# Performance work log

Measured on AMD Instinct MI355X. Metric: run time of the kernel, lower is better.

## Reference

```python
import jax, jax.numpy as jnp
import numpy as np

L = 2          # conv layers
N = 50000      # nodes
E = 800000     # edges (before self loops)
F_IN = 256     # raw node features
C = 32         # embed features (out_channels per head)
H = 4          # heads
HC = H * C
ED = 1         # edge feature dim
EPS = 1e-5
NEG_SLOPE = 0.2


def _xavier(k, shape):
    fan_in, fan_out = shape[-2], shape[-1]
    lim = float(np.sqrt(6.0 / (fan_in + fan_out)))
    return jax.random.uniform(k, shape, jnp.float32, -lim, lim)


def setup_inputs() -> dict:
    key = jax.random.key(0)
    ks = jax.random.split(key, 12)
    x = jax.random.normal(ks[0], (N, F_IN), jnp.float32)
    src = jax.random.randint(ks[1], (E,), 0, N, dtype=jnp.int32)
    off = jax.random.randint(ks[2], (E,), 1, N, dtype=jnp.int32)
    dst = (src + off) % N  # guarantees no pre-existing self loops (PyG removes then re-adds them)
    edge_index = jnp.stack([src, dst])
    edge_attr = jax.random.normal(ks[3], (E, ED), jnp.float32)
    return {
        "x": x,
        "edge_index": edge_index,
        "edge_attr": edge_attr,
        "W_emb": _xavier(ks[4], (F_IN, C)),
        "b_emb": jnp.zeros((C,), jnp.float32),
        "ln0_w": jnp.ones((C,), jnp.float32),
        "ln0_b": jnp.zeros((C,), jnp.float32),
        "Wl": _xavier(ks[5], (L, C, HC)),
        "bl": jnp.zeros((L, HC), jnp.float32),
        "Wr": _xavier(ks[6], (L, C, HC)),
        "br": jnp.zeros((L, HC), jnp.float32),
        "We": _xavier(ks[7], (L, ED, HC)),
        "att": jax.random.normal(ks[8], (L, H, C), jnp.float32) * 0.1,
        "gat_b": jnp.zeros((L, HC), jnp.float32),
        "ln1_w": jnp.ones((L, HC), jnp.float32),
        "ln1_b": jnp.zeros((L, HC), jnp.float32),
        "lin_w": _xavier(ks[9], (L, HC, C)),
        "lin_b": jnp.zeros((L, C), jnp.float32),
        "ln2_w": jnp.ones((L, C), jnp.float32),
        "ln2_b": jnp.zeros((L, C), jnp.float32),
    }


def _node_ln(x, w, b):
    # torch.nn.LayerNorm over last dim
    mu = jnp.mean(x, axis=-1, keepdims=True)
    xc = x - mu
    var = jnp.mean(xc * xc, axis=-1, keepdims=True)
    return xc / jnp.sqrt(var + EPS) * w + b


def _graph_ln(x, w, b):
    # torch_geometric.nn.norm.LayerNorm, mode='graph': normalize over ALL nodes+features
    mu = jnp.mean(x)
    xc = x - mu
    var = jnp.mean(xc * xc)
    return xc / jnp.sqrt(var + EPS) * w + b


def _gatv2_layer(h, src, dst, ea, Wl, bl, Wr, br, We, att, gat_b):
    n = h.shape[0]
    xl = (h @ Wl + bl).reshape(n, H, C)   # lin_l(x) -> source transform
    xr = (h @ Wr + br).reshape(n, H, C)   # lin_r(x) -> target transform
    e = (ea @ We).reshape(-1, H, C)       # lin_edge(edge_attr), no bias
    z = jax.nn.leaky_relu(xl[src] + xr[dst] + e, NEG_SLOPE)   # [Etot,H,C]
    logits = jnp.einsum("ehc,hc->eh", z, att)                  # [Etot,H]
    # segment softmax over destination nodes (every node has a self loop)
    m = jax.ops.segment_max(logits, dst, num_segments=n)
    ex = jnp.exp(logits - m[dst])
    s = jax.ops.segment_sum(ex, dst, num_segments=n)
    alpha = ex / s[dst]                                        # [Etot,H]
    msg = alpha[..., None] * xl[src]                           # [Etot,H,C]
    out = jax.ops.segment_sum(msg, dst, num_segments=n)        # [N,H,C]
    return out.reshape(n, HC) + gat_b


def reference(x, edge_index, edge_attr, W_emb, b_emb, ln0_w, ln0_b, Wl, bl, Wr, br,
              We, att, gat_b, ln1_w, ln1_b, lin_w, lin_b, ln2_w, ln2_b):
    n = x.shape[0]
    loop = jnp.arange(n, dtype=edge_index.dtype)
    src = jnp.concatenate([edge_index[0], loop])
    dst = jnp.concatenate([edge_index[1], loop])
    ea = jnp.concatenate([edge_attr, jnp.zeros((n, edge_attr.shape[1]), edge_attr.dtype)])  # fill_value=0.0

    # node_embed: Dropout(eval=identity) -> Linear -> LayerNorm -> ReLU
    h = jax.nn.relu(_node_ln(x @ W_emb + b_emb, ln0_w, ln0_b))
    hs = [h]
    for i in range(L):
        g = _gatv2_layer(h, src, dst, ea, Wl[i], bl[i], Wr[i], br[i], We[i], att[i], gat_b[i])
        g = jax.nn.relu(_graph_ln(g, ln1_w[i], ln1_b[i]))     # PyG graph-mode LayerNorm + ReLU
        g = g @ lin_w[i] + lin_b[i]                            # heads>1 projection back to C
        h = jax.nn.relu(_node_ln(g, ln2_w[i], ln2_b[i]))
        hs.append(h)
    # JumpingKnowledge mode='max': elementwise max over layer outputs
    return jnp.max(jnp.stack(hs, axis=0), axis=0)
```

## Files before the change

kernel.cpp:

```cpp
#include <hip/hip_runtime.h>
#include <hip/hip_fp16.h>

constexpr int kNodes = 50000;
constexpr int kNE    = 800000;
constexpr int kFin   = 256;
constexpr int kC     = 32;
constexpr int kH     = 4;
constexpr int kHC    = 128;
constexpr int kTN    = 16;
constexpr int kLWP   = 130;
constexpr int kEmbedBlocks = kNodes / kTN;
constexpr int kTransBlocks = (kNodes + 31) / 32;
constexpr int kHistGS = 256;
constexpr int kReoGS  = 256;
constexpr int kDegBlocks = (kNodes + 255) / 256;
constexpr float kEps   = 1e-5f;
constexpr float kSlope = 0.2f;
constexpr float kL2E   = 1.44269504f;
constexpr float kShift2 = 8.0f * 1.44269504f;

typedef _Float16 f16;
typedef _Float16 f16x2 __attribute__((ext_vector_type(2)));
struct alignas(16) h8 { f16x2 v[4]; };

__device__ __forceinline__ float fdot2_(f16x2 a, f16x2 b, float c) {
#if __has_builtin(__builtin_amdgcn_fdot2)
    return __builtin_amdgcn_fdot2(a, b, c, false);
#else
    return fmaf((float)a.x, (float)b.x, fmaf((float)a.y, (float)b.y, c));
#endif
}

template<int CTRL>
__device__ __forceinline__ float dpp_add(float v) {
    int x = __builtin_amdgcn_update_dpp(0, __float_as_int(v), CTRL, 0xF, 0xF, true);
    return v + __int_as_float(x);
}
__device__ __forceinline__ float red8(float p) {
    p = dpp_add<0xB1>(p);
    p = dpp_add<0x4E>(p);
    p = dpp_add<0x141>(p);
    return p;
}

__global__ void __launch_bounds__(256) k_prep(
    unsigned* __restrict__ deg, const float* __restrict__ W, f16* __restrict__ Wh) {
    int t = threadIdx.x;
    if (blockIdx.x < kDegBlocks) {
        int i = blockIdx.x * 256 + t;
        if (i < kNodes) deg[i] = 0u;
        return;
    }
    int i = (blockIdx.x - kDegBlocks) * 256 + t;
    int k = i >> 5, c = i & 31;
    Wh[((k >> 3) * kC + c) * 8 + (k & 7)] = (f16)W[i];
}

__global__ void __launch_bounds__(256) k_embed_hist(
    const float* __restrict__ x, const f16* __restrict__ Wh, const float* __restrict__ b,
    const float* __restrict__ lnw, const float* __restrict__ lnb,
    float* __restrict__ h, float* __restrict__ jk,
    const int* __restrict__ dst, int* __restrict__ deg, unsigned short* __restrict__ rank) {
    __shared__ f16 sxh[kTN * kFin];
    __shared__ f16 sWh[kFin / 8 * kC * 8];
    int t = threadIdx.x;
    if (blockIdx.x < kHistGS) {
        const int stride = kHistGS * 256;
        int e = blockIdx.x * 256 + t;
        for (; e + 3 * stride < kNE; e += 4 * stride) {
            int d0 = dst[e], d1 = dst[e + stride], d2 = dst[e + 2 * stride], d3 = dst[e + 3 * stride];
            int r0 = atomicAdd(&deg[d0], 1);
            int r1 = atomicAdd(&deg[d1], 1);
            int r2 = atomicAdd(&deg[d2], 1);
            int r3 = atomicAdd(&deg[d3], 1);
            rank[e] = (unsigned short)r0;
            rank[e + stride] = (unsigned short)r1;
            rank[e + 2 * stride] = (unsigned short)r2;
            rank[e + 3 * stride] = (unsigned short)r3;
        }
        for (; e < kNE; e += stride) {
            int d = dst[e];
            rank[e] = (unsigned short)atomicAdd(&deg[d], 1);
        }
        return;
    }
    int n0 = (blockIdx.x - kHistGS) * kTN;
    {
        const h8* Wg = (const h8*)Wh;
        h8* sW8 = (h8*)sWh;
        for (int i = t; i < kFin * kC / 8; i += 256) sW8[i] = Wg[i];
    }
    const float2* xg2 = (const float2*)(x + (long)n0 * kFin);
    f16x2* sx2 = (f16x2*)sxh;
    for (int i = t; i < kTN * kFin / 2; i += 256) {
        float2 v = xg2[i];
        f16x2 hv; hv.x = (f16)v.x; hv.y = (f16)v.y;
        sx2[i] = hv;
    }
    __syncthreads();
    int c = t & 31, n2 = t >> 5;
    const h8* xa = (const h8*)(sxh + n2 * kFin);
    const h8* xb = (const h8*)(sxh + (n2 + 8) * kFin);
    const h8* wr = (const h8*)sWh;
    float a0 = 0.f, a0b = 0.f, a1 = 0.f, a1b = 0.f;
    #pragma unroll 8
    for (int i8 = 0; i8 < kFin / 8; ++i8) {
        h8 xv0 = xa[i8];
        h8 xv1 = xb[i8];
        h8 wv  = wr[i8 * kC + c];
        a0  = fdot2_(xv0.v[0], wv.v[0], a0);
        a0b = fdot2_(xv0.v[1], wv.v[1], a0b);
        a0  = fdot2_(xv0.v[2], wv.v[2], a0);
        a0b = fdot2_(xv0.v[3], wv.v[3], a0b);
        a1  = fdot2_(xv1.v[0], wv.v[0], a1);
        a1b = fdot2_(xv1.v[1], wv.v[1], a1b);
        a1  = fdot2_(xv1.v[2], wv.v[2], a1);
        a1b = fdot2_(xv1.v[3], wv.v[3], a1b);
    }
    float acc0 = a0 + a0b, acc1 = a1 + a1b;
    float bc = b[c], lw = lnw[c], lb = lnb[c];
    {
        float y = acc0 + bc;
        float m = y;
        #pragma unroll
        for (int o = 1; o < 32; o <<= 1) m += __shfl_xor(m, o);
        m *= (1.f / kC);
        float xc = y - m, v = xc * xc;
        #pragma unroll
        for (int o = 1; o < 32; o <<= 1) v += __shfl_xor(v, o);
        v *= (1.f / kC);
        float out = fmaxf(xc * rsqrtf(v + kEps) * lw + lb, 0.f);
        int node = n0 + n2;
        h[node * kC + c] = out;
        jk[node * kC + c] = out;
    }
    {
        float y = acc1 + bc;
        float m = y;
        #pragma unroll
        for (int o = 1; o < 32; o <<= 1) m += __shfl_xor(m, o);
        m *= (1.f / kC);
        float xc = y - m, v = xc * xc;
        #pragma unroll
        for (int o = 1; o < 32; o <<= 1) v += __shfl_xor(v, o);
        v *= (1.f / kC);
        float out = fmaxf(xc * rsqrtf(v + kEps) * lw + lb, 0.f);
        int node = n0 + n2 + 8;
        h[node * kC + c] = out;
        jk[node * kC + c] = out;
    }
}

__device__ __forceinline__ void trans_body(
    int bid, float* s_h, const float* __restrict__ h,
    const float* __restrict__ Wl, const float* __restrict__ bl,
    const float* __restrict__ Wr, const float* __restrict__ br,
    __half* __restrict__ xl, float* __restrict__ xr) {
    int t = threadIdx.x;
    int j = t & 127, hf = t >> 7;
    float wl[kC], wr[kC];
    #pragma unroll
    for (int k = 0; k < kC; ++k) { wl[k] = Wl[k * kHC + j]; wr[k] = Wr[k * kHC + j]; }
    float blj = bl[j], brj = br[j];
    int n0 = bid * 32;
    int nn = min(32, kNodes - n0);
    for (int i = t; i < nn * kC; i += 256) s_h[i] = h[n0 * kC + i];
    __syncthreads();
    int nend = min(nn, hf * 16 + 16);
    for (int n = hf * 16; n < nend; ++n) {
        const float4* h4 = (const float4*)(s_h + n * kC);
        float al = blj, ar = brj;
        #pragma unroll
        for (int kq = 0; kq < 8; ++kq) {
            float4 hv = h4[kq];
            al += hv.x * wl[kq*4] + hv.y * wl[kq*4+1] + hv.z * wl[kq*4+2] + hv.w * wl[kq*4+3];
            ar += hv.x * wr[kq*4] + hv.y * wr[kq*4+1] + hv.z * wr[kq*4+2] + hv.w * wr[kq*4+3];
        }
        long g = (long)(n0 + n) * kHC + j;
        xl[g] = __float2half(al);
        xr[g] = ar;
    }
}

__global__ void __launch_bounds__(256) k_trans(
    const float* __restrict__ h,
    const float* __restrict__ Wl, const float* __restrict__ bl,
    const float* __restrict__ Wr, const float* __restrict__ br,
    __half* __restrict__ xl, float* __restrict__ xr, float* __restrict__ stats) {
    __shared__ float s_h[32 * kC];
    if (blockIdx.x == 0 && threadIdx.x == 0) { stats[0] = 0.f; stats[1] = 0.f; }
    trans_body(blockIdx.x, s_h, h, Wl, bl, Wr, br, xl, xr);
}

__global__ void __launch_bounds__(256) k_trans_reorder(
    const float* __restrict__ h,
    const float* __restrict__ Wl, const float* __restrict__ bl,
    const float* __restrict__ Wr, const float* __restrict__ br,
    __half* __restrict__ xl, float* __restrict__ xr,
    const int* __restrict__ src, const int* __restrict__ dst, const float* __restrict__ ea,
    const int* __restrict__ rowptr, const unsigned short* __restrict__ rank,
    int2* __restrict__ epack, float* __restrict__ stats) {
    __shared__ float s_h[32 * kC];
    if (blockIdx.x < kReoGS) {
        const int stride = kReoGS * 256;
        int e = blockIdx.x * 256 + threadIdx.x;
        for (; e + 3 * stride < kNE; e += 4 * stride) {
            int e1 = e + stride, e2 = e + 2 * stride, e3 = e + 3 * stride;
            int d0 = dst[e], d1 = dst[e1], d2 = dst[e2], d3 = dst[e3];
            int r0 = rank[e], r1 = rank[e1], r2 = rank[e2], r3 = rank[e3];
            int p0 = rowptr[d0] + r0, p1 = rowptr[d1] + r1;
            int p2 = rowptr[d2] + r2, p3 = rowptr[d3] + r3;
            epack[p0] = make_int2(src[e],  __float_as_int(ea[e]));
            epack[p1] = make_int2(src[e1], __float_as_int(ea[e1]));
            epack[p2] = make_int2(src[e2], __float_as_int(ea[e2]));
            epack[p3] = make_int2(src[e3], __float_as_int(ea[e3]));
        }
        for (; e < kNE; e += stride) {
            int d = dst[e];
            int pos = rowptr[d] + (int)rank[e];
            epack[pos] = make_int2(src[e], __float_as_int(ea[e]));
        }
        return;
    }
    if (blockIdx.x == kReoGS && threadIdx.x == 0) { stats[0] = 0.f; stats[1] = 0.f; }
    trans_body(blockIdx.x - kReoGS, s_h, h, Wl, bl, Wr, br, xl, xr);
}

__global__ void __launch_bounds__(256) k_scan1(const int* __restrict__ deg,
                                               int* __restrict__ excl, int* __restrict__ bsum) {
    __shared__ int s[256];
    int t = threadIdx.x;
    int i = blockIdx.x * 256 + t;
    int v = (i < kNodes) ? deg[i] : 0;
    s[t] = v;
    __syncthreads();
    for (int o = 1; o < 256; o <<= 1) {
        int tv = (t >= o) ? s[t - o] : 0;
        __syncthreads();
        s[t] += tv;
        __syncthreads();
    }
    if (i < kNodes) excl[i] = s[t] - v;
    if (t == 255) bsum[blockIdx.x] = s[255];
}

__global__ void __launch_bounds__(256) k_scan2(int* __restrict__ bsum, int nb) {
    __shared__ int s[256];
    int t = threadIdx.x;
    int v = (t < nb) ? bsum[t] : 0;
    s[t] = v;
    __syncthreads();
    for (int o = 1; o < 256; o <<= 1) {
        int tv = (t >= o) ? s[t - o] : 0;
        __syncthreads();
        s[t] += tv;
        __syncthreads();
    }
    if (t < nb) bsum[t] = s[t];
}

__global__ void __launch_bounds__(256) k_scan3(int* __restrict__ excl, const int* __restrict__ bsum) {
    int i = blockIdx.x * 256 + threadIdx.x;
    if (i >= kNodes) return;
    if (blockIdx.x > 0) excl[i] += bsum[blockIdx.x - 1];
}

struct h4 { __half2 a, b; };
template<int U>
__device__ __forceinline__ void gat_batch(
    const int2* __restrict__ epack, int base2, bool slot0, int f,
    const h4* __restrict__ xl4, float4 Wev, float4 xrv, float4 av,
    float& l, float& o0, float& o1, float& o2, float& o3) {
    int2 pa[U], pb[U];
    #pragma unroll
    for (int u = 0; u < U; ++u) {
        pa[u] = epack[base2 + 2 * u];
        pb[u] = epack[base2 + 2 * u + 1];
    }
    h4 xv[U]; float eav[U];
    #pragma unroll
    for (int u = 0; u < U; ++u) {
        int srow = slot0 ? pa[u].x : pb[u].x;
        xv[u] = xl4[(long)srow * 32 + f];
        eav[u] = __int_as_float(slot0 ? pa[u].y : pb[u].y);
    }
    #pragma unroll
    for (int u = 0; u < U; ++u) {
        float2 x01 = __half22float2(xv[u].a), x23 = __half22float2(xv[u].b);
        float a0 = fmaf(eav[u], Wev.x, xrv.x) + x01.x;
        float a1 = fmaf(eav[u], Wev.y, xrv.y) + x01.y;
        float a2 = fmaf(eav[u], Wev.z, xrv.z) + x23.x;
        float a3 = fmaf(eav[u], Wev.w, xrv.w) + x23.y;
        a0 = fmaxf(a0, kSlope * a0); a1 = fmaxf(a1, kSlope * a1);
        a2 = fmaxf(a2, kSlope * a2); a3 = fmaxf(a3, kSlope * a3);
        float pp = red8(a0 * av.x + a1 * av.y + a2 * av.z + a3 * av.w);
        float eu = __builtin_amdgcn_exp2f(pp - kShift2);
        l += eu;
        o0 = fmaf(eu, x01.x, o0); o1 = fmaf(eu, x01.y, o1);
        o2 = fmaf(eu, x23.x, o2); o3 = fmaf(eu, x23.y, o3);
    }
}

__global__ void __launch_bounds__(256) k_edge(
    const int* __restrict__ rowptr, const int* __restrict__ deg,
    const int2* __restrict__ epack,
    const __half* __restrict__ xl, float* __restrict__ xrg,
    const float* __restrict__ We, const float* __restrict__ att,
    const float* __restrict__ gat_b, float* __restrict__ ps, float* __restrict__ pq) {
    int t = threadIdx.x & 63;
    int w = __builtin_amdgcn_readfirstlane(threadIdx.x >> 6);
    int d = blockIdx.x * 4 + w;
    int f = t & 31;
    bool slot0 = (t < 32);
    float em0 = slot0 ? 1.f : 0.f;

    const h4* xl4 = (const h4*)xl;
    long rowq = (long)d * 32;

    float4 xrv = ((const float4*)xrg)[rowq + f];
    float4 Wev = ((const float4*)We)[f];
    float4 av  = ((const float4*)att)[f];
    av.x *= kL2E; av.y *= kL2E; av.z *= kL2E; av.w *= kL2E;
    float4 gb  = ((const float4*)gat_b)[f];

    h4 xs = xl4[rowq + f];
    float2 xs01 = __half22float2(xs.a), xs23 = __half22float2(xs.b);

    float z0 = xs01.x + xrv.x, z1 = xs01.y + xrv.y;
    float z2 = xs23.x + xrv.z, z3 = xs23.y + xrv.w;
    z0 = fmaxf(z0, kSlope * z0); z1 = fmaxf(z1, kSlope * z1);
    z2 = fmaxf(z2, kSlope * z2); z3 = fmaxf(z3, kSlope * z3);
    float p = red8(z0 * av.x + z1 * av.y + z2 * av.z + z3 * av.w);
    float ee = __builtin_amdgcn_exp2f(p - kShift2) * em0;
    float l = ee;
    float o0 = ee * xs01.x, o1 = ee * xs01.y, o2 = ee * xs23.x, o3 = ee * xs23.y;

    int base = rowptr[d], cnt = deg[d];
    int npair = cnt >> 1;
    int e = 0;
    for (; e + 8 <= npair; e += 8)
        gat_batch<8>(epack, base + 2 * e, slot0, f, xl4, Wev, xrv, av, l, o0, o1, o2, o3);
    if (e + 4 <= npair) {
        gat_batch<4>(epack, base + 2 * e, slot0, f, xl4, Wev, xrv, av, l, o0, o1, o2, o3);
        e += 4;
    }
    for (; e < npair; ++e)
        gat_batch<1>(epack, base + 2 * e, slot0, f, xl4, Wev, xrv, av, l, o0, o1, o2, o3);
    if (cnt & 1) {
        int2 ep = epack[base + cnt - 1];
        int srow = ep.x;
        float eav = __int_as_float(ep.y);
        h4 xv = xl4[(long)srow * 32 + f];
        float2 x01 = __half22float2(xv.a), x23 = __half22float2(xv.b);
        float a0 = fmaf(eav, Wev.x, xrv.x) + x01.x;
        float a1 = fmaf(eav, Wev.y, xrv.y) + x01.y;
        float a2 = fmaf(eav, Wev.z, xrv.z) + x23.x;
        float a3 = fmaf(eav, Wev.w, xrv.w) + x23.y;
        a0 = fmaxf(a0, kSlope * a0); a1 = fmaxf(a1, kSlope * a1);
        a2 = fmaxf(a2, kSlope * a2); a3 = fmaxf(a3, kSlope * a3);
        float pp = red8(a0 * av.x + a1 * av.y + a2 * av.z + a3 * av.w);
        float eu = __builtin_amdgcn_exp2f(pp - kShift2) * em0;
        l += eu;
        o0 = fmaf(eu, x01.x, o0); o1 = fmaf(eu, x01.y, o1);
        o2 = fmaf(eu, x23.x, o2); o3 = fmaf(eu, x23.y, o3);
    }
    l  += __shfl_xor(l, 32);
    o0 += __shfl_xor(o0, 32); o1 += __shfl_xor(o1, 32);
    o2 += __shfl_xor(o2, 32); o3 += __shfl_xor(o3, 32);
    float rl = __builtin_amdgcn_rcpf(l);
    float v0 = o0 * rl, v1 = o1 * rl, v2 = o2 * rl, v3 = o3 * rl;
    if (slot0)
        ((float4*)xrg)[rowq + f] = make_float4(v0, v1, v2, v3);
    float vb0 = v0 + gb.x, vb1 = v1 + gb.y, vb2 = v2 + gb.z, vb3 = v3 + gb.w;
    float s = vb0 + vb1 + vb2 + vb3;
    float q = vb0 * vb0 + vb1 * vb1 + vb2 * vb2 + vb3 * vb3;
    #pragma unroll
    for (int mm = 1; mm < 32; mm <<= 1) { s += __shfl_xor(s, mm); q += __shfl_xor(q, mm); }
    if (t == 0) { ps[d] = s; pq[d] = q; }
}

__global__ void __launch_bounds__(1024) k_statsr(
    const float* __restrict__ ps, const float* __restrict__ pq, float* __restrict__ stats) {
    __shared__ float rs[1024], rq[1024];
    int t = threadIdx.x;
    float s = 0.f, q = 0.f;
    for (int i = blockIdx.x * 1024 + t; i < kNodes; i += 8 * 1024) { s += ps[i]; q += pq[i]; }
    rs[t] = s; rq[t] = q;
    __syncthreads();
    for (int o = 512; o > 0; o >>= 1) {
        if (t < o) { rs[t] += rs[t + o]; rq[t] += rq[t + o]; }
        __syncthreads();
    }
    if (t == 0) { atomicAdd(&stats[0], rs[0]); atomicAdd(&stats[1], rq[0]); }
}

__global__ void __launch_bounds__(256) k_post(
    const float* __restrict__ g, const float* __restrict__ gat_b,
    const float* __restrict__ ln1w, const float* __restrict__ ln1b,
    const float* __restrict__ linw, const float* __restrict__ linb,
    const float* __restrict__ ln2w, const float* __restrict__ ln2b,
    const float* __restrict__ stats, const float* __restrict__ jk_in,
    float* __restrict__ h, float* __restrict__ jk_out) {
    __shared__ float s_lwT[kC * kLWP];
    __shared__ float s_vb[8 * kHC];
    int t = threadIdx.x;
    int n0 = blockIdx.x * 8;
    const float inv = 1.f / ((float)kNodes * kHC);
    float mean = stats[0] * inv;
    float var  = stats[1] * inv - mean * mean;
    float rstd = rsqrtf(var + kEps);
    for (int i = t; i < kHC * kC; i += 256) {
        int k = i >> 5, c = i & 31;
        s_lwT[c * kLWP + k] = linw[i];
    }
    for (int i = t; i < 8 * kHC; i += 256) {
        int node = n0 + (i >> 7), f = i & 127;
        float a = (g[(long)node * kHC + f] + gat_b[f] - mean) * rstd * ln1w[f] + ln1b[f];
        s_vb[i] = fmaxf(a, 0.f);
    }
    __syncthreads();
    int n = t >> 5, c = t & 31;
    int node = n0 + n;
    float acc = linb[c];
    const float* vb = s_vb + n * kHC;
    const float* wr = s_lwT + c * kLWP;
    #pragma unroll 8
    for (int k = 0; k < kHC; k += 4) {
        float4 v4 = *(const float4*)(vb + k);
        float2 w0 = *(const float2*)(wr + k);
        float2 w1 = *(const float2*)(wr + k + 2);
        acc += v4.x * w0.x + v4.y * w0.y + v4.z * w1.x + v4.w * w1.y;
    }
    float m = acc;
    #pragma unroll
    for (int mm = 1; mm < 32; mm <<= 1) m += __shfl_xor(m, mm);
    m *= (1.f / kC);
    float dd = acc - m;
    float q = dd * dd;
    #pragma unroll
    for (int mm = 1; mm < 32; mm <<= 1) q += __shfl_xor(q, mm);
    q *= (1.f / kC);
    float out = dd * rsqrtf(q + kEps) * ln2w[c] + ln2b[c];
    out = fmaxf(out, 0.f);
    h[node * kC + c] = out;
    jk_out[node * kC + c] = fmaxf(jk_in[node * kC + c], out);
}

extern "C" void kernel_launch(void* const* d_in, const int* in_sizes, int n_in,
                              void* d_out, int out_size, void* d_ws, size_t ws_size,
                              hipStream_t stream) {
    (void)in_sizes; (void)n_in; (void)out_size; (void)ws_size;
    const float* x     = (const float*)d_in[0];
    const int*   ei    = (const int*)d_in[1];
    const int*   src   = ei;
    const int*   dst   = ei + kNE;
    const float* ea    = (const float*)d_in[2];
    const float* W_emb = (const float*)d_in[3];
    const float* b_emb = (const float*)d_in[4];
    const float* ln0w  = (const float*)d_in[5];
    const float* ln0b  = (const float*)d_in[6];
    const float* Wl    = (const float*)d_in[7];
    const float* bl    = (const float*)d_in[8];
    const float* Wr    = (const float*)d_in[9];
    const float* br    = (const float*)d_in[10];
    const float* We    = (const float*)d_in[11];
    const float* att   = (const float*)d_in[12];
    const float* gat_b = (const float*)d_in[13];
    const float* ln1w  = (const float*)d_in[14];
    const float* ln1b  = (const float*)d_in[15];
    const float* linw  = (const float*)d_in[16];
    const float* linb  = (const float*)d_in[17];
    const float* ln2w  = (const float*)d_in[18];
    const float* ln2b  = (const float*)d_in[19];

    char* wsb = (char*)d_ws;
    float*  h      = (float*)(wsb);
    float*  jk     = (float*)(wsb +  6400000);
    float*  xrg    = (float*)(wsb + 12800000);
    __half* xl     = (__half*)(wsb + 38400000);
    int2*   epack  = (int2*)(wsb + 51200000);
    int*    deg    = (int*)(wsb + 57600000);
    int*    rowptr = (int*)(wsb + 58000000);
    int*    bsum   = (int*)(wsb + 58200000);
    float*  stats  = (float*)(wsb + 58201024);
    float*  ps     = (float*)(wsb + 58300000);
    float*  pq     = (float*)(wsb + 58500000);
    unsigned short* rank = (unsigned short*)(wsb + 58700000);
    f16*    Wh     = (f16*)(wsb + 60400000);

    const int scanBlocks = (kNodes + 255) / 256;
    const int edgeBlocks = kNodes / 4;
    const int postBlocks = kNodes / 8;

    hipLaunchKernelGGL(k_prep, dim3(kDegBlocks + 32), dim3(256), 0, stream,
                       (unsigned*)deg, W_emb, Wh);
    hipLaunchKernelGGL(k_embed_hist, dim3(kHistGS + kEmbedBlocks), dim3(256), 0, stream,
                       x, Wh, b_emb, ln0w, ln0b, h, jk, dst, deg, rank);
    hipLaunchKernelGGL(k_scan1, dim3(scanBlocks), dim3(256), 0, stream, deg, rowptr, bsum);
    hipLaunchKernelGGL(k_scan2, dim3(1), dim3(256), 0, stream, bsum, scanBlocks);
    hipLaunchKernelGGL(k_scan3, dim3(scanBlocks), dim3(256), 0, stream, rowptr, bsum);
    hipLaunchKernelGGL(k_trans_reorder, dim3(kReoGS + kTransBlocks), dim3(256), 0, stream,
                       h, Wl, bl, Wr, br, xl, xrg,
                       src, dst, ea, rowptr, rank, epack, stats);
    for (int l = 0; l < 2; ++l) {
        if (l == 1) {
            hipLaunchKernelGGL(k_trans, dim3(kTransBlocks), dim3(256), 0, stream,
                               h, Wl + l * kC * kHC, bl + l * kHC,
                               Wr + l * kC * kHC, br + l * kHC, xl, xrg, stats);
        }
        hipLaunchKernelGGL(k_edge, dim3(edgeBlocks), dim3(256), 0, stream,
                           rowptr, deg, epack, xl, xrg,
                           We + l * kHC, att + l * kH * kC, gat_b + l * kHC, ps, pq);
        hipLaunchKernelGGL(k_statsr, dim3(8), dim3(1024), 0, stream, ps, pq, stats);
        hipLaunchKernelGGL(k_post, dim3(postBlocks), dim3(256), 0, stream,
                           xrg, gat_b + l * kHC, ln1w + l * kHC, ln1b + l * kHC,
                           linw + l * kHC * kC, linb + l * kC,
                           ln2w + l * kC, ln2b + l * kC, stats, jk,
                           h, (l == 1) ? (float*)d_out : jk);
    }
}
```

Measured before the change: 418.9 us.

## Fuse layer-1 node transform into post kernel and collapse scan into one kernel

The layer-1 xl/xr projection moves into the tail of the layer-0 k_post kernel. It is computed from the freshly normalized node values held in shared memory, so the separate k_trans launch and the h write and re-read go away. The three-kernel prefix scan becomes a single 1024-thread block in which each thread scans a contiguous chunk serially. Graph-LN stats now use separate slots per layer and are zeroed once in k_prep. The cost is a single-CU scan with uncoalesced chunked loads and more register pressure in k_post from the per-thread weight arrays.

```diff
diff --git a/kernel.cpp b/kernel.cpp
--- a/kernel.cpp
+++ b/kernel.cpp
@@ -44,8 +44,10 @@
 }
 
 __global__ void __launch_bounds__(256) k_prep(
-    unsigned* __restrict__ deg, const float* __restrict__ W, f16* __restrict__ Wh) {
+    unsigned* __restrict__ deg, const float* __restrict__ W, f16* __restrict__ Wh,
+    float* __restrict__ stats) {
     int t = threadIdx.x;
+    if (blockIdx.x == 0 && t < 4) stats[t] = 0.f;
     if (blockIdx.x < kDegBlocks) {
         int i = blockIdx.x * 256 + t;
         if (i < kNodes) deg[i] = 0u;
@@ -182,16 +184,6 @@
     }
 }
 
-__global__ void __launch_bounds__(256) k_trans(
-    const float* __restrict__ h,
-    const float* __restrict__ Wl, const float* __restrict__ bl,
-    const float* __restrict__ Wr, const float* __restrict__ br,
-    __half* __restrict__ xl, float* __restrict__ xr, float* __restrict__ stats) {
-    __shared__ float s_h[32 * kC];
-    if (blockIdx.x == 0 && threadIdx.x == 0) { stats[0] = 0.f; stats[1] = 0.f; }
-    trans_body(blockIdx.x, s_h, h, Wl, bl, Wr, br, xl, xr);
-}
-
 __global__ void __launch_bounds__(256) k_trans_reorder(
     const float* __restrict__ h,
     const float* __restrict__ Wl, const float* __restrict__ bl,
@@ -199,7 +191,7 @@
     __half* __restrict__ xl, float* __restrict__ xr,
     const int* __restrict__ src, const int* __restrict__ dst, const float* __restrict__ ea,
     const int* __restrict__ rowptr, const unsigned short* __restrict__ rank,
-    int2* __restrict__ epack, float* __restrict__ stats) {
+    int2* __restrict__ epack) {
     __shared__ float s_h[32 * kC];
     if (blockIdx.x < kReoGS) {
         const int stride = kReoGS * 256;
@@ -222,47 +214,30 @@
         }
         return;
     }
-    if (blockIdx.x == kReoGS && threadIdx.x == 0) { stats[0] = 0.f; stats[1] = 0.f; }
     trans_body(blockIdx.x - kReoGS, s_h, h, Wl, bl, Wr, br, xl, xr);
 }
 
-__global__ void __launch_bounds__(256) k_scan1(const int* __restrict__ deg,
-                                               int* __restrict__ excl, int* __restrict__ bsum) {
-    __shared__ int s[256];
+__global__ void __launch_bounds__(1024) k_scan(
+    const int* __restrict__ deg, int* __restrict__ rowptr) {
+    __shared__ int s[1024];
+    const int CH = (kNodes + 1023) / 1024;
     int t = threadIdx.x;
-    int i = blockIdx.x * 256 + t;
-    int v = (i < kNodes) ? deg[i] : 0;
-    s[t] = v;
+    int lo = t * CH, hi = min(lo + CH, kNodes);
+    int sum = 0;
+    for (int i = lo; i < hi; ++i) sum += deg[i];
+    s[t] = sum;
     __syncthreads();
-    for (int o = 1; o < 256; o <<= 1) {
-        int tv = (t >= o) ? s[t - o] : 0;
+    for (int o = 1; o < 1024; o <<= 1) {
+        int v = (t >= o) ? s[t - o] : 0;
         __syncthreads();
-        s[t] += tv;
+        s[t] += v;
         __syncthreads();
     }
-    if (i < kNodes) excl[i] = s[t] - v;
-    if (t == 255) bsum[blockIdx.x] = s[255];
-}
-
-__global__ void __launch_bounds__(256) k_scan2(int* __restrict__ bsum, int nb) {
-    __shared__ int s[256];
-    int t = threadIdx.x;
-    int v = (t < nb) ? bsum[t] : 0;
-    s[t] = v;
-    __syncthreads();
-    for (int o = 1; o < 256; o <<= 1) {
-        int tv = (t >= o) ? s[t - o] : 0;
-        __syncthreads();
-        s[t] += tv;
-        __syncthreads();
-    }
-    if (t < nb) bsum[t] = s[t];
-}
-
-__global__ void __launch_bounds__(256) k_scan3(int* __restrict__ excl, const int* __restrict__ bsum) {
-    int i = blockIdx.x * 256 + threadIdx.x;
-    if (i >= kNodes) return;
-    if (blockIdx.x > 0) excl[i] += bsum[blockIdx.x - 1];
+    int off = (t > 0) ? s[t - 1] : 0;
+    for (int i = lo; i < hi; ++i) {
+        rowptr[i] = off;
+        off += deg[i];
+    }
 }
 
 struct h4 { __half2 a, b; };
@@ -400,11 +375,21 @@
     const float* __restrict__ linw, const float* __restrict__ linb,
     const float* __restrict__ ln2w, const float* __restrict__ ln2b,
     const float* __restrict__ stats, const float* __restrict__ jk_in,
-    float* __restrict__ h, float* __restrict__ jk_out) {
+    float* __restrict__ jk_out, int do_trans,
+    const float* __restrict__ Wl, const float* __restrict__ bl,
+    const float* __restrict__ Wr, const float* __restrict__ br,
+    __half* __restrict__ xl, float* __restrict__ xr) {
     __shared__ float s_lwT[kC * kLWP];
     __shared__ float s_vb[8 * kHC];
+    __shared__ float s_hh[8 * kC];
     int t = threadIdx.x;
     int n0 = blockIdx.x * 8;
+    int j = t & 127;
+    float wl[kC], wr[kC];
+    if (do_trans) {
+        #pragma unroll
+        for (int k = 0; k < kC; ++k) { wl[k] = Wl[k * kHC + j]; wr[k] = Wr[k * kHC + j]; }
+    }
     const float inv = 1.f / ((float)kNodes * kHC);
     float mean = stats[0] * inv;
     float var  = stats[1] * inv - mean * mean;
@@ -423,12 +408,12 @@
     int node = n0 + n;
     float acc = linb[c];
     const float* vb = s_vb + n * kHC;
-    const float* wr = s_lwT + c * kLWP;
+    const float* wrt = s_lwT + c * kLWP;
     #pragma unroll 8
     for (int k = 0; k < kHC; k += 4) {
         float4 v4 = *(const float4*)(vb + k);
-        float2 w0 = *(const float2*)(wr + k);
-        float2 w1 = *(const float2*)(wr + k + 2);
+        float2 w0 = *(const float2*)(wrt + k);
+        float2 w1 = *(const float2*)(wrt + k + 2);
         acc += v4.x * w0.x + v4.y * w0.y + v4.z * w1.x + v4.w * w1.y;
     }
     float m = acc;
@@ -442,8 +427,27 @@
     q *= (1.f / kC);
     float out = dd * rsqrtf(q + kEps) * ln2w[c] + ln2b[c];
     out = fmaxf(out, 0.f);
-    h[node * kC + c] = out;
     jk_out[node * kC + c] = fmaxf(jk_in[node * kC + c], out);
+    if (!do_trans) return;
+    s_hh[n * kC + c] = out;
+    __syncthreads();
+    int hf = t >> 7;
+    float blj = bl[j], brj = br[j];
+    #pragma unroll
+    for (int nn2 = 0; nn2 < 4; ++nn2) {
+        int nn = hf * 4 + nn2;
+        const float4* h4p = (const float4*)(s_hh + nn * kC);
+        float al = blj, ar = brj;
+        #pragma unroll
+        for (int kq = 0; kq < 8; ++kq) {
+            float4 hv = h4p[kq];
+            al += hv.x * wl[kq*4] + hv.y * wl[kq*4+1] + hv.z * wl[kq*4+2] + hv.w * wl[kq*4+3];
+            ar += hv.x * wr[kq*4] + hv.y * wr[kq*4+1] + hv.z * wr[kq*4+2] + hv.w * wr[kq*4+3];
+        }
+        long gg = (long)(n0 + nn) * kHC + j;
+        xl[gg] = __float2half(al);
+        xr[gg] = ar;
+    }
 }
 
 extern "C" void kernel_launch(void* const* d_in, const int* in_sizes, int n_in,
@@ -481,41 +485,35 @@
     int2*   epack  = (int2*)(wsb + 51200000);
     int*    deg    = (int*)(wsb + 57600000);
     int*    rowptr = (int*)(wsb + 58000000);
-    int*    bsum   = (int*)(wsb + 58200000);
     float*  stats  = (float*)(wsb + 58201024);
     float*  ps     = (float*)(wsb + 58300000);
     float*  pq     = (float*)(wsb + 58500000);
     unsigned short* rank = (unsigned short*)(wsb + 58700000);
     f16*    Wh     = (f16*)(wsb + 60400000);
 
-    const int scanBlocks = (kNodes + 255) / 256;
     const int edgeBlocks = kNodes / 4;
     const int postBlocks = kNodes / 8;
 
     hipLaunchKernelGGL(k_prep, dim3(kDegBlocks + 32), dim3(256), 0, stream,
-                       (unsigned*)deg, W_emb, Wh);
+                       (unsigned*)deg, W_emb, Wh, stats);
     hipLaunchKernelGGL(k_embed_hist, dim3(kHistGS + kEmbedBlocks), dim3(256), 0, stream,
                        x, Wh, b_emb, ln0w, ln0b, h, jk, dst, deg, rank);
-    hipLaunchKernelGGL(k_scan1, dim3(scanBlocks), dim3(256), 0, stream, deg, rowptr, bsum);
-    hipLaunchKernelGGL(k_scan2, dim3(1), dim3(256), 0, stream, bsum, scanBlocks);
-    hipLaunchKernelGGL(k_scan3, dim3(scanBlocks), dim3(256), 0, stream, rowptr, bsum);
+    hipLaunchKernelGGL(k_scan, dim3(1), dim3(1024), 0, stream, deg, rowptr);
     hipLaunchKernelGGL(k_trans_reorder, dim3(kReoGS + kTransBlocks), dim3(256), 0, stream,
                        h, Wl, bl, Wr, br, xl, xrg,
-                       src, dst, ea, rowptr, rank, epack, stats);
+                       src, dst, ea, rowptr, rank, epack);
     for (int l = 0; l < 2; ++l) {
-        if (l == 1) {
-            hipLaunchKernelGGL(k_trans, dim3(kTransBlocks), dim3(256), 0, stream,
-                               h, Wl + l * kC * kHC, bl + l * kHC,
-                               Wr + l * kC * kHC, br + l * kHC, xl, xrg, stats);
-        }
         hipLaunchKernelGGL(k_edge, dim3(edgeBlocks), dim3(256), 0, stream,
                            rowptr, deg, epack, xl, xrg,
                            We + l * kHC, att + l * kH * kC, gat_b + l * kHC, ps, pq);
-        hipLaunchKernelGGL(k_statsr, dim3(8), dim3(1024), 0, stream, ps, pq, stats);
+        hipLaunchKernelGGL(k_statsr, dim3(8), dim3(1024), 0, stream, ps, pq, stats + 2 * l);
         hipLaunchKernelGGL(k_post, dim3(postBlocks), dim3(256), 0, stream,
                            xrg, gat_b + l * kHC, ln1w + l * kHC, ln1b + l * kHC,
                            linw + l * kHC * kC, linb + l * kC,
-                           ln2w + l * kC, ln2b + l * kC, stats, jk,
-                           h, (l == 1) ? (float*)d_out : jk);
-    }
-}
+                           ln2w + l * kC, ln2b + l * kC, stats + 2 * l, jk,
+                           (l == 1) ? (float*)d_out : jk,
+                           (l == 0) ? 1 : 0,
+                           Wl + kC * kHC, bl + kHC, Wr + kC * kHC, br + kHC,
+                           xl, xrg);
+    }
+}
```

Result: slower. 485.3 us (+15.9%).
